# Optimization experiments

Measured on AMD Instinct MI355X. Metric: run time of the kernel, lower is better.

The kernel has to match this reference:

```python
import jax, jax.numpy as jnp
import numpy as np

N_TOK, BATCH, D, MEM, H, W = 196, 64, 256, 2048, 16, 16


def setup_inputs() -> dict:
    key = jax.random.key(0)
    ks = jax.random.split(key, 9)
    w_scale = 1.0 / np.sqrt(D)  # ~ Linear default init scale
    return {
        "input_tokens": jax.random.normal(ks[0], (N_TOK, BATCH, D), jnp.float32),
        "ch_memory": jax.random.normal(ks[1], (MEM, D), jnp.float32) * 0.1,
        "ch_wq": jax.random.normal(ks[2], (D, D), jnp.float32) * w_scale,
        "ch_wk": jax.random.normal(ks[3], (D, D), jnp.float32) * w_scale,
        "ch_wv": jax.random.normal(ks[4], (D, D), jnp.float32) * w_scale,
        "sp_memory": jax.random.normal(ks[5], (MEM, H, W), jnp.float32) * 0.1,
        "sp_wq": jax.random.normal(ks[6], (D, D), jnp.float32) * w_scale,
        "sp_wk": jax.random.normal(ks[7], (D, D), jnp.float32) * w_scale,
        "sp_wv": jax.random.normal(ks[8], (D, D), jnp.float32) * w_scale,
    }


def reference(input_tokens, ch_memory, ch_wq, ch_wk, ch_wv,
              sp_memory, sp_wq, sp_wk, sp_wv):
    n_tok, batch, d = input_tokens.shape
    hw = d  # spatial branch requires feature_dim == H*W
    x = input_tokens.reshape(n_tok * batch, d)  # [NB, D]

    # ---- Channel memory branch: dot-product softmax read ----
    q = x @ ch_wq.T                       # [NB, D]
    k = ch_memory @ ch_wk.T               # [M, D]
    v = ch_memory @ ch_wv.T               # [M, D]
    scores = (q @ k.T) * (1.0 / jnp.sqrt(jnp.float32(d)))  # [NB, M]
    att_c = jax.nn.softmax(scores, axis=-1)
    out_c = att_c @ v                     # [NB, D]

    # ---- Spatial memory branch: SSIM-score softmax read ----
    mem_flat = sp_memory.reshape(sp_memory.shape[0], hw)  # [M, HW]
    qf = x @ sp_wq.T                      # [NB, HW]
    kf = mem_flat @ sp_wk.T               # [M, HW]
    vf = mem_flat @ sp_wv.T               # [M, HW]

    q_mean = jnp.mean(qf, axis=1, keepdims=True)          # [NB, 1]
    k_mean = jnp.mean(kf, axis=1, keepdims=True)          # [M, 1]
    q_var = jnp.var(qf, axis=1, ddof=1, keepdims=True)    # unbiased, like torch.var
    k_var = jnp.var(kf, axis=1, ddof=1, keepdims=True)
    cov = ((qf - q_mean) @ (kf - k_mean).T) / jnp.float32(hw - 1)  # [NB, M]

    c1, c2 = 0.01, 0.03
    mean_prod = q_mean @ k_mean.T                          # [NB, M]
    numerator = (2.0 * mean_prod + c1) * (2.0 * cov + c2)
    denominator = (q_mean ** 2 + (k_mean.T) ** 2 + c1) * (q_var + k_var.T + c2)
    ssim = numerator / (denominator + 1e-8)                # [NB, M]

    att_s = jax.nn.softmax(ssim, axis=-1)
    out_s = att_s @ vf                     # [NB, HW] == [NB, D]

    return (out_c + out_s).reshape(n_tok, batch, d)
```

## Files before the change

kernel.cpp:

```cpp
#include <hip/hip_runtime.h>

#define NBQ 12544
#define DM  256
#define MM  2048

typedef __attribute__((ext_vector_type(8)))  __bf16 bf16x8;
typedef __attribute__((ext_vector_type(4)))  float  floatx4;

__device__ __forceinline__ ushort f2bf(float x) {
    unsigned u = __float_as_uint(x);
    u += 0x7fffu + ((u >> 16) & 1u);
    return (ushort)(u >> 16);
}
__device__ __forceinline__ float bf2f(ushort h) {
    return __uint_as_float(((unsigned)h) << 16);
}
__device__ __forceinline__ ushort4 cvt4(float4 f) {
    union { __bf16 h[4]; ushort4 u; } r;
    r.h[0] = (__bf16)f.x; r.h[1] = (__bf16)f.y;
    r.h[2] = (__bf16)f.z; r.h[3] = (__bf16)f.w;
    return r.u;
}

__device__ __forceinline__ void glds16(const ushort* g, ushort* l) {
    __builtin_amdgcn_global_load_lds(
        (const __attribute__((address_space(1))) unsigned int*)g,
        (__attribute__((address_space(3))) unsigned int*)l, 16, 0, 0);
}

#define WAITVM(N) asm volatile("s_waitcnt vmcnt(" #N ")" ::: "memory")
#define WAITLGKM0 asm volatile("s_waitcnt lgkmcnt(0)" ::: "memory")

__global__ __launch_bounds__(256) void gemm_proj_all(
    const float* __restrict__ x,      const float* __restrict__ ch_mem,
    const float* __restrict__ ch_wq,  const float* __restrict__ ch_wk,
    const float* __restrict__ ch_wv,  const float* __restrict__ sp_mem,
    const float* __restrict__ sp_wq,  const float* __restrict__ sp_wk,
    const float* __restrict__ sp_wv,
    ushort* __restrict__ Qb,  ushort* __restrict__ QFb,
    ushort* __restrict__ Kb,  ushort* __restrict__ KFb,
    ushort* __restrict__ Vtb, ushort* __restrict__ VFtb)
{
    __shared__ ushort As[64][72];
    __shared__ ushort W1s[64][72];
    __shared__ ushort W2s[64][72];

    int bid = blockIdx.x;
    const float* A; const float* W1; const float* W2;
    ushort* C1; ushort* C2; int nrows, trans2;
    if (bid < 784) {
        A = x; W1 = ch_wq; W2 = sp_wq; C1 = Qb; C2 = QFb; nrows = NBQ; trans2 = 0;
    } else if (bid < 912) {
        A = ch_mem; W1 = ch_wk; W2 = ch_wv; C1 = Kb; C2 = Vtb;
        nrows = MM; trans2 = 1; bid -= 784;
    } else {
        A = sp_mem; W1 = sp_wk; W2 = sp_wv; C1 = KFb; C2 = VFtb;
        nrows = MM; trans2 = 1; bid -= 912;
    }
    const int r0 = (bid >> 2) * 64;
    const int c0 = (bid & 3) * 64;

    const int tid  = threadIdx.x;
    const int wv   = tid >> 6;
    const int lane = tid & 63;
    const int quad = lane >> 4;
    const int l16  = lane & 15;
    const int rw = (wv & 1) * 32;
    const int cw = (wv >> 1) * 32;

    floatx4 acc1[2][2], acc2[2][2];
    #pragma unroll
    for (int i = 0; i < 2; ++i)
        #pragma unroll
        for (int j = 0; j < 2; ++j) {
            acc1[i][j] = (floatx4){0.f, 0.f, 0.f, 0.f};
            acc2[i][j] = (floatx4){0.f, 0.f, 0.f, 0.f};
        }

    float4 a4[4], w14[4], w24[4];
    #pragma unroll
    for (int it = 0; it < 4; ++it) {
        int idx = tid + it * 256;
        int r = idx >> 4, c4 = (idx & 15) * 4;
        a4[it]  = *(const float4*)(A  + (size_t)(r0 + r) * 256 + c4);
        w14[it] = *(const float4*)(W1 + (size_t)(c0 + r) * 256 + c4);
        w24[it] = *(const float4*)(W2 + (size_t)(c0 + r) * 256 + c4);
    }

    for (int d0 = 0; d0 < 256; d0 += 64) {
        __syncthreads();
        #pragma unroll
        for (int it = 0; it < 4; ++it) {
            int idx = tid + it * 256;
            int r = idx >> 4, c4 = (idx & 15) * 4;
            *(ushort4*)&As[r][c4]  = cvt4(a4[it]);
            *(ushort4*)&W1s[r][c4] = cvt4(w14[it]);
            *(ushort4*)&W2s[r][c4] = cvt4(w24[it]);
        }
        if (d0 + 64 < 256) {
            #pragma unroll
            for (int it = 0; it < 4; ++it) {
                int idx = tid + it * 256;
                int r = idx >> 4, c4 = (idx & 15) * 4;
                a4[it]  = *(const float4*)(A  + (size_t)(r0 + r) * 256 + d0 + 64 + c4);
                w14[it] = *(const float4*)(W1 + (size_t)(c0 + r) * 256 + d0 + 64 + c4);
                w24[it] = *(const float4*)(W2 + (size_t)(c0 + r) * 256 + d0 + 64 + c4);
            }
        }
        __syncthreads();
        #pragma unroll
        for (int kk = 0; kk < 64; kk += 32) {
            bf16x8 aA0 = *(const bf16x8*)&As[rw + l16][kk + quad * 8];
            bf16x8 aA1 = *(const bf16x8*)&As[rw + 16 + l16][kk + quad * 8];
            bf16x8 b10 = *(const bf16x8*)&W1s[cw + l16][kk + quad * 8];
            bf16x8 b11 = *(const bf16x8*)&W1s[cw + 16 + l16][kk + quad * 8];
            bf16x8 b20 = *(const bf16x8*)&W2s[cw + l16][kk + quad * 8];
            bf16x8 b21 = *(const bf16x8*)&W2s[cw + 16 + l16][kk + quad * 8];
            acc1[0][0] = __builtin_amdgcn_mfma_f32_16x16x32_bf16(aA0, b10, acc1[0][0], 0, 0, 0);
            acc1[0][1] = __builtin_amdgcn_mfma_f32_16x16x32_bf16(aA0, b11, acc1[0][1], 0, 0, 0);
            acc1[1][0] = __builtin_amdgcn_mfma_f32_16x16x32_bf16(aA1, b10, acc1[1][0], 0, 0, 0);
            acc1[1][1] = __builtin_amdgcn_mfma_f32_16x16x32_bf16(aA1, b11, acc1[1][1], 0, 0, 0);
            acc2[0][0] = __builtin_amdgcn_mfma_f32_16x16x32_bf16(aA0, b20, acc2[0][0], 0, 0, 0);
            acc2[0][1] = __builtin_amdgcn_mfma_f32_16x16x32_bf16(aA0, b21, acc2[0][1], 0, 0, 0);
            acc2[1][0] = __builtin_amdgcn_mfma_f32_16x16x32_bf16(aA1, b20, acc2[1][0], 0, 0, 0);
            acc2[1][1] = __builtin_amdgcn_mfma_f32_16x16x32_bf16(aA1, b21, acc2[1][1], 0, 0, 0);
        }
    }

    #pragma unroll
    for (int ag = 0; ag < 2; ++ag)
        #pragma unroll
        for (int cg = 0; cg < 2; ++cg)
            #pragma unroll
            for (int i = 0; i < 4; ++i)
                C1[(size_t)(r0 + rw + ag * 16 + quad * 4 + i) * 256
                   + c0 + cw + cg * 16 + l16] = f2bf(acc1[ag][cg][i]);

    if (!trans2) {
        #pragma unroll
        for (int ag = 0; ag < 2; ++ag)
            #pragma unroll
            for (int cg = 0; cg < 2; ++cg)
                #pragma unroll
                for (int i = 0; i < 4; ++i)
                    C2[(size_t)(r0 + rw + ag * 16 + quad * 4 + i) * 256
                       + c0 + cw + cg * 16 + l16] = f2bf(acc2[ag][cg][i]);
    } else {
        __syncthreads();
        #pragma unroll
        for (int ag = 0; ag < 2; ++ag)
            #pragma unroll
            for (int cg = 0; cg < 2; ++cg)
                #pragma unroll
                for (int i = 0; i < 4; ++i)
                    W2s[cw + cg * 16 + l16][rw + ag * 16 + quad * 4 + i] = f2bf(acc2[ag][cg][i]);
        __syncthreads();
        const int col = tid >> 2;
        const int seg = (tid & 3) * 16;
        #pragma unroll
        for (int j = 0; j < 2; ++j)
            *(uint4*)(C2 + (size_t)(c0 + col) * nrows + r0 + seg + j * 8) =
                *(const uint4*)&W2s[col][seg + j * 8];
    }
}

__global__ __launch_bounds__(256) void row_stats_kf(
    const ushort* __restrict__ KFb, float* __restrict__ km, float* __restrict__ kv)
{
    const int row  = blockIdx.x * 4 + (threadIdx.x >> 6);
    const int lane = threadIdx.x & 63;
    ushort4 u = *(const ushort4*)(KFb + (size_t)row * 256 + lane * 4);
    float a = bf2f(u.x), b = bf2f(u.y), c = bf2f(u.z), d = bf2f(u.w);
    float s  = a + b + c + d;
    float ss = a * a + b * b + c * c + d * d;
    #pragma unroll
    for (int off = 32; off > 0; off >>= 1) {
        s  += __shfl_down(s, off);
        ss += __shfl_down(ss, off);
    }
    if (lane == 0) {
        float m = s * (1.f / 256.f);
        km[row] = m;
        kv[row] = (ss - 256.f * m * m) * (1.f / 255.f) + 0.03f;
    }
}

#define STAGE_TILE(b, ti)                                                     \
    {                                                                         \
        const ushort* kp_ = kp0 + (size_t)(ti) * 32 * DM;                     \
        const ushort* vp_ = vp0 + (ti) * 32;                                  \
        ushort* dst_ = SMu + (b) * 16384;                                     \
        _Pragma("unroll")                                                     \
        for (int p = 0; p < 4; ++p) {                                         \
            int db = (wv * 4 + p) * 512;                                      \
            glds16(kp_ + offK[p], dst_ + db);                                 \
            glds16(vp_ + offV[p], dst_ + 8192 + db);                          \
        }                                                                     \
    }

__global__ __launch_bounds__(256, 2) void fused_attn_x4(
    const ushort* __restrict__ Qb,  const ushort* __restrict__ QFb,
    const ushort* __restrict__ Kb,  const ushort* __restrict__ KFb,
    const ushort* __restrict__ Vtb, const ushort* __restrict__ VFtb,
    const float* __restrict__ km_, const float* __restrict__ kv_,
    float* __restrict__ part, float* __restrict__ denp)
{
    __shared__ ushort SMu[32768];

    const int tid  = threadIdx.x;
    const int wv   = tid >> 6;
    const int lane = tid & 63;
    const int quad = lane >> 4;
    const int l16  = lane & 15;

    const int k8   = blockIdx.x & 7;
    const int j    = blockIdx.x >> 3;
    const int br   = (j >= 49) ? 1 : 0;
    const int half = k8 & 3;
    const int qc   = (k8 >> 2) * 49 + (br ? j - 49 : j);
    const int q0   = qc * 128;
    const int kbase = half * 512;
    const int NT   = 16;

    const ushort* qsrc = br ? QFb : Qb;
    const ushort* Ksel = br ? KFb : Kb;
    const ushort* Vsel = br ? VFtb : Vtb;

    bf16x8 aQ0[8], aQ1[8];
    {
        const ushort* qp = qsrc + (size_t)(q0 + wv * 32 + l16) * DM + quad * 8;
        #pragma unroll
        for (int s = 0; s < 8; ++s) {
            aQ0[s] = __builtin_nontemporal_load((const bf16x8*)(qp + s * 32));
            aQ1[s] = __builtin_nontemporal_load((const bf16x8*)(qp + 16 * DM + s * 32));
        }
    }

    float qmv0 = 0.f, qvv0 = 0.f, qmv1 = 0.f, qvv1 = 0.f, qm2_0 = 0.f, qm2_1 = 0.f;
    if (br) {
        float s0 = 0.f, ss0 = 0.f, s1 = 0.f, ss1 = 0.f;
        #pragma unroll
        for (int s = 0; s < 8; ++s)
            #pragma unroll
            for (int jj = 0; jj < 8; ++jj) {
                float v0 = (float)aQ0[s][jj], v1 = (float)aQ1[s][jj];
                s0 += v0; ss0 += v0 * v0; s1 += v1; ss1 += v1 * v1;
            }
        s0  += __shfl_xor(s0, 16, 64);  s0  += __shfl_xor(s0, 32, 64);
        ss0 += __shfl_xor(ss0, 16, 64); ss0 += __shfl_xor(ss0, 32, 64);
        s1  += __shfl_xor(s1, 16, 64);  s1  += __shfl_xor(s1, 32, 64);
        ss1 += __shfl_xor(ss1, 16, 64); ss1 += __shfl_xor(ss1, 32, 64);
        qmv0 = s0 * (1.f / 256.f);
        qvv0 = (ss0 - 256.f * qmv0 * qmv0) * (1.f / 255.f);
        qmv1 = s1 * (1.f / 256.f);
        qvv1 = (ss1 - 256.f * qmv1 * qmv1) * (1.f / 255.f);
        qm2_0 = qmv0 * qmv0 + 0.01f;
        qm2_1 = qmv1 * qmv1 + 0.01f;
    }

    int offK[4], offV[4];
    #pragma unroll
    for (int p = 0; p < 4; ++p) {
        int jw = wv * 4 + p;
        int Rk = 2 * jw + (lane >> 5);
        int rk = (Rk & 3) + ((Rk >> 4) & 1) * 4 + ((Rk >> 2) & 3) * 8;
        int ck = (lane & 31) ^ (Rk & 7);
        offK[p] = rk * DM + ck * 8;
        int Rv = 16 * jw + (lane >> 2);
        int cv = (lane & 3) ^ (Rv & 3);
        offV[p] = Rv * MM + cv * 8;
    }

    const ushort* kp0 = Ksel + (size_t)kbase * DM;
    const ushort* vp0 = Vsel + kbase;

    floatx4 acc0[16], acc1[16];
    #pragma unroll
    for (int t = 0; t < 16; ++t) {
        acc0[t] = (floatx4){0.f, 0.f, 0.f, 0.f};
        acc1[t] = (floatx4){0.f, 0.f, 0.f, 0.f};
    }
    float den0 = 0.f, den1 = 0.f;
    const int ksw  = l16 & 7;
    const int vswo = (quad ^ (l16 & 3)) * 8;

    floatx4 kmc0 = {0,0,0,0}, kmc1 = {0,0,0,0}, kvc0 = {0,0,0,0}, kvc1 = {0,0,0,0};

    STAGE_TILE(0, 0);
    if (br) {
        kmc0 = *(const floatx4*)(km_ + kbase + 8 * quad);
        kmc1 = *(const floatx4*)(km_ + kbase + 8 * quad + 4);
        kvc0 = *(const floatx4*)(kv_ + kbase + 8 * quad);
        kvc1 = *(const floatx4*)(kv_ + kbase + 8 * quad + 4);
    }

    int buf = 0;
    for (int ti = 0; ti < NT; ++ti) {
        const bool have_next = (ti + 1 < NT);
        floatx4 kmn0 = {0,0,0,0}, kmn1 = {0,0,0,0}, kvn0 = {0,0,0,0}, kvn1 = {0,0,0,0};
        if (have_next) {
            STAGE_TILE(buf ^ 1, ti + 1);
            if (br) {
                const int kk1 = kbase + (ti + 1) * 32;
                kmn0 = *(const floatx4*)(km_ + kk1 + 8 * quad);
                kmn1 = *(const floatx4*)(km_ + kk1 + 8 * quad + 4);
                kvn0 = *(const floatx4*)(kv_ + kk1 + 8 * quad);
                kvn1 = *(const floatx4*)(kv_ + kk1 + 8 * quad + 4);
            }
        }
        if (have_next) { if (br) WAITVM(12); else WAITVM(8); }
        else           { WAITVM(0); }
        __builtin_amdgcn_sched_barrier(0);
        __builtin_amdgcn_s_barrier();
        __builtin_amdgcn_sched_barrier(0);

        const ushort* Ks = SMu + buf * 16384;
        const ushort* Vs = Ks + 8192;

        floatx4 S00 = (floatx4){0.f, 0.f, 0.f, 0.f};
        floatx4 S10 = (floatx4){0.f, 0.f, 0.f, 0.f};
        floatx4 S01 = (floatx4){0.f, 0.f, 0.f, 0.f};
        floatx4 S11 = (floatx4){0.f, 0.f, 0.f, 0.f};
        #pragma unroll
        for (int s = 0; s < 8; ++s) {
            int off = ((s * 4 + quad) ^ ksw) * 8;
            bf16x8 aK0 = *(const bf16x8*)(Ks + l16 * DM + off);
            bf16x8 aK1 = *(const bf16x8*)(Ks + 4096 + l16 * DM + off);
            S00 = __builtin_amdgcn_mfma_f32_16x16x32_bf16(aK0, aQ0[s], S00, 0, 0, 0);
            S10 = __builtin_amdgcn_mfma_f32_16x16x32_bf16(aK1, aQ0[s], S10, 0, 0, 0);
            S01 = __builtin_amdgcn_mfma_f32_16x16x32_bf16(aK0, aQ1[s], S01, 0, 0, 0);
            S11 = __builtin_amdgcn_mfma_f32_16x16x32_bf16(aK1, aQ1[s], S11, 0, 0, 0);
        }

        float p0[8], p1[8];
        if (!br) {
            #pragma unroll
            for (int r = 0; r < 4; ++r) {
                p0[r]     = __expf(S00[r] * 0.0625f);
                p0[4 + r] = __expf(S10[r] * 0.0625f);
                p1[r]     = __expf(S01[r] * 0.0625f);
                p1[4 + r] = __expf(S11[r] * 0.0625f);
            }
        } else {
            #pragma unroll
            for (int r = 0; r < 4; ++r) {
                {
                    float kmr = kmc0[r];
                    float mp  = qmv0 * kmr;
                    float cov = (S00[r] - 256.f * mp) * (1.f / 255.f);
                    float num = (2.f * mp + 0.01f) * (2.f * cov + 0.03f);
                    float dn  = (qm2_0 + kmr * kmr) * (qvv0 + kvc0[r]) + 1e-8f;
                    p0[r] = __expf(num / dn);
                }
                {
                    float kmr = kmc1[r];
                    float mp  = qmv0 * kmr;
                    float cov = (S10[r] - 256.f * mp) * (1.f / 255.f);
                    float num = (2.f * mp + 0.01f) * (2.f * cov + 0.03f);
                    float dn  = (qm2_0 + kmr * kmr) * (qvv0 + kvc1[r]) + 1e-8f;
                    p0[4 + r] = __expf(num / dn);
                }
                {
                    float kmr = kmc0[r];
                    float mp  = qmv1 * kmr;
                    float cov = (S01[r] - 256.f * mp) * (1.f / 255.f);
                    float num = (2.f * mp + 0.01f) * (2.f * cov + 0.03f);
                    float dn  = (qm2_1 + kmr * kmr) * (qvv1 + kvc0[r]) + 1e-8f;
                    p1[r] = __expf(num / dn);
                }
                {
                    float kmr = kmc1[r];
                    float mp  = qmv1 * kmr;
                    float cov = (S11[r] - 256.f * mp) * (1.f / 255.f);
                    float num = (2.f * mp + 0.01f) * (2.f * cov + 0.03f);
                    float dn  = (qm2_1 + kmr * kmr) * (qvv1 + kvc1[r]) + 1e-8f;
                    p1[4 + r] = __expf(num / dn);
                }
            }
        }
        union { __bf16 h[8]; bf16x8 v; } ap0, ap1;
        #pragma unroll
        for (int jj = 0; jj < 8; ++jj) {
            den0 += p0[jj]; ap0.h[jj] = (__bf16)p0[jj];
            den1 += p1[jj]; ap1.h[jj] = (__bf16)p1[jj];
        }

        #pragma unroll
        for (int t = 0; t < 16; ++t) {
            bf16x8 bV = *(const bf16x8*)(Vs + (t * 16 + l16) * 32 + vswo);
            acc0[t] = __builtin_amdgcn_mfma_f32_16x16x32_bf16(ap0.v, bV, acc0[t], 0, 0, 0);
            acc1[t] = __builtin_amdgcn_mfma_f32_16x16x32_bf16(ap1.v, bV, acc1[t], 0, 0, 0);
        }

        WAITLGKM0;
        __builtin_amdgcn_sched_barrier(0);
        __builtin_amdgcn_s_barrier();
        __builtin_amdgcn_sched_barrier(0);

        kmc0 = kmn0; kmc1 = kmn1; kvc0 = kvn0; kvc1 = kvn1;
        buf ^= 1;
    }

    den0 += __shfl_xor(den0, 16, 64); den0 += __shfl_xor(den0, 32, 64);
    den1 += __shfl_xor(den1, 16, 64); den1 += __shfl_xor(den1, 32, 64);

    const int sec = br * 4 + half;
    float* Np = part + (size_t)sec * ((size_t)NBQ * DM);
    #pragma unroll
    for (int t = 0; t < 16; ++t)
        #pragma unroll
        for (int r = 0; r < 4; ++r) {
            int row = q0 + wv * 32 + quad * 4 + r;
            __builtin_nontemporal_store(acc0[t][r], &Np[(size_t)row * DM + t * 16 + l16]);
            __builtin_nontemporal_store(acc1[t][r], &Np[(size_t)(row + 16) * DM + t * 16 + l16]);
        }
    if (lane < 16) {
        denp[(size_t)sec * NBQ + q0 + wv * 32 + lane]      = den0;
        denp[(size_t)sec * NBQ + q0 + wv * 32 + 16 + lane] = den1;
    }
}

__global__ __launch_bounds__(256, 2) void fused_attn_fb(
    const ushort* __restrict__ Qb,  const ushort* __restrict__ QFb,
    const ushort* __restrict__ Kb,  const ushort* __restrict__ KFb,
    const ushort* __restrict__ Vtb, const ushort* __restrict__ VFtb,
    const float* __restrict__ km_, const float* __restrict__ kv_,
    float* __restrict__ out)
{
    __shared__ ushort SMu[32768];
    float* combuf = (float*)SMu;

    const int tid  = threadIdx.x;
    const int wv   = tid >> 6;
    const int lane = tid & 63;
    const int quad = lane >> 4;
    const int l16  = lane & 15;
    const int qsel = wv & 1;
    const int br   = wv >> 1;
    const int q0   = blockIdx.x * 32;

    const ushort* qsrc = br ? QFb : Qb;
    bf16x8 aQ[8];
    {
        const ushort* qp = qsrc + (size_t)(q0 + qsel * 16 + l16) * DM + quad * 8;
        #pragma unroll
        for (int s = 0; s < 8; ++s) aQ[s] = *(const bf16x8*)(qp + s * 32);
    }

    float qmv = 0.f, qvv = 0.f, qm2 = 0.f;
    if (br) {
        float sum = 0.f, ss = 0.f;
        #pragma unroll
        for (int s = 0; s < 8; ++s)
            #pragma unroll
            for (int jj = 0; jj < 8; ++jj) {
                float v = (float)aQ[s][jj];
                sum += v; ss += v * v;
            }
        sum += __shfl_xor(sum, 16, 64); sum += __shfl_xor(sum, 32, 64);
        ss  += __shfl_xor(ss, 16, 64);  ss  += __shfl_xor(ss, 32, 64);
        qmv = sum * (1.f / 256.f);
        qvv = (ss - 256.f * qmv * qmv) * (1.f / 255.f);
        qm2 = qmv * qmv + 0.01f;
    }

    int offK[4], offV[4];
    #pragma unroll
    for (int p = 0; p < 4; ++p) {
        int jw = wv * 4 + p;
        int Rk = 2 * jw + (lane >> 5);
        int rk = (Rk & 3) + ((Rk >> 4) & 1) * 4 + ((Rk >> 2) & 3) * 8;
        int ck = (lane & 31) ^ (Rk & 7);
        offK[p] = rk * DM + ck * 8;
        int Rv = 16 * jw + (lane >> 2);
        int cv = (lane & 3) ^ (Rv & 3);
        offV[p] = Rv * MM + cv * 8;
    }

    const ushort* kp  = Kb;
    const ushort* kfp = KFb;
    const ushort* vp  = Vtb;
    const ushort* vfp = VFtb;

    floatx4 acc[16];
    #pragma unroll
    for (int t = 0; t < 16; ++t) acc[t] = (floatx4){0.f, 0.f, 0.f, 0.f};
    float den = 0.f;

    const int ksw  = l16 & 7;
    const int vswo = (quad ^ (l16 & 3)) * 8;

    for (int kt = 0; kt < MM; kt += 32) {
        __syncthreads();
        #pragma unroll
        for (int p = 0; p < 4; ++p) {
            int db = (wv * 4 + p) * 512;
            glds16(kp  + offK[p], SMu + db);
            glds16(kfp + offK[p], SMu + 8192 + db);
            glds16(vp  + offV[p], SMu + 16384 + db);
            glds16(vfp + offV[p], SMu + 24576 + db);
        }
        kp += 32 * DM; kfp += 32 * DM; vp += 32; vfp += 32;
        __syncthreads();

        const ushort* Ks = SMu + (br ? 8192 : 0);
        floatx4 S0 = (floatx4){0.f, 0.f, 0.f, 0.f};
        floatx4 S1 = (floatx4){0.f, 0.f, 0.f, 0.f};
        #pragma unroll
        for (int s = 0; s < 8; ++s) {
            int off = ((s * 4 + quad) ^ ksw) * 8;
            bf16x8 aK0 = *(const bf16x8*)(Ks + l16 * DM + off);
            bf16x8 aK1 = *(const bf16x8*)(Ks + 4096 + l16 * DM + off);
            S0 = __builtin_amdgcn_mfma_f32_16x16x32_bf16(aK0, aQ[s], S0, 0, 0, 0);
            S1 = __builtin_amdgcn_mfma_f32_16x16x32_bf16(aK1, aQ[s], S1, 0, 0, 0);
        }

        float pb[8];
        if (!br) {
            #pragma unroll
            for (int r = 0; r < 4; ++r) {
                pb[r]     = __expf(S0[r] * 0.0625f);
                pb[4 + r] = __expf(S1[r] * 0.0625f);
            }
        } else {
            floatx4 km0 = *(const floatx4*)(km_ + kt + 8 * quad);
            floatx4 km1 = *(const floatx4*)(km_ + kt + 8 * quad + 4);
            floatx4 kv0 = *(const floatx4*)(kv_ + kt + 8 * quad);
            floatx4 kv1 = *(const floatx4*)(kv_ + kt + 8 * quad + 4);
            #pragma unroll
            for (int r = 0; r < 4; ++r) {
                {
                    float kmr = km0[r];
                    float mp  = qmv * kmr;
                    float cov = (S0[r] - 256.f * mp) * (1.f / 255.f);
                    float num = (2.f * mp + 0.01f) * (2.f * cov + 0.03f);
                    float dn  = (qm2 + kmr * kmr) * (qvv + kv0[r]) + 1e-8f;
                    pb[r] = __expf(num / dn);
                }
                {
                    float kmr = km1[r];
                    float mp  = qmv * kmr;
                    float cov = (S1[r] - 256.f * mp) * (1.f / 255.f);
                    float num = (2.f * mp + 0.01f) * (2.f * cov + 0.03f);
                    float dn  = (qm2 + kmr * kmr) * (qvv + kv1[r]) + 1e-8f;
                    pb[4 + r] = __expf(num / dn);
                }
            }
        }
        union { __bf16 h[8]; bf16x8 v; } ap;
        #pragma unroll
        for (int jj = 0; jj < 8; ++jj) {
            den += pb[jj];
            ap.h[jj] = (__bf16)pb[jj];
        }

        const ushort* Vs = SMu + (br ? 24576 : 16384);
        #pragma unroll
        for (int t = 0; t < 16; ++t) {
            bf16x8 bV = *(const bf16x8*)(Vs + (t * 16 + l16) * 32 + vswo);
            acc[t] = __builtin_amdgcn_mfma_f32_16x16x32_bf16(ap.v, bV, acc[t], 0, 0, 0);
        }
    }

    den += __shfl_xor(den, 16, 64);
    den += __shfl_xor(den, 32, 64);
    float rdn[4];
    #pragma unroll
    for (int r = 0; r < 4; ++r)
        rdn[r] = 1.f / __shfl(den, quad * 4 + r, 64);

    __syncthreads();
    if (br) {
        #pragma unroll
        for (int t = 0; t < 16; ++t)
            #pragma unroll
            for (int r = 0; r < 4; ++r)
                combuf[(qsel * 16 + quad * 4 + r) * 256 + t * 16 + l16] = acc[t][r] * rdn[r];
    }
    __syncthreads();
    if (!br) {
        #pragma unroll
        for (int t = 0; t < 16; ++t)
            #pragma unroll
            for (int r = 0; r < 4; ++r) {
                int ql = qsel * 16 + quad * 4 + r;
                out[(size_t)(q0 + ql) * DM + t * 16 + l16] =
                    acc[t][r] * rdn[r] + combuf[ql * 256 + t * 16 + l16];
            }
    }
}

__global__ __launch_bounds__(256) void combine_halves(
    const float* __restrict__ part, const float* __restrict__ denp,
    float* __restrict__ out)
{
    const size_t stride = (size_t)NBQ * 64;
    const floatx4* p4 = (const floatx4*)part;
    floatx4* o4 = (floatx4*)out;
    #pragma unroll
    for (int u = 0; u < 2; ++u) {
        size_t i = (size_t)blockIdx.x * 512 + (size_t)u * 256 + threadIdx.x;
        int q = (int)(i >> 6);
        float dc = 0.f, ds = 0.f;
        #pragma unroll
        for (int h = 0; h < 4; ++h) {
            dc += denp[(size_t)h * NBQ + q];
            ds += denp[(size_t)(4 + h) * NBQ + q];
        }
        float rc = 1.f / dc, rs = 1.f / ds;
        floatx4 nc = {0.f, 0.f, 0.f, 0.f}, ns = {0.f, 0.f, 0.f, 0.f};
        #pragma unroll
        for (int h = 0; h < 4; ++h) {
            floatx4 c = __builtin_nontemporal_load(&p4[(size_t)h * stride + i]);
            floatx4 s = __builtin_nontemporal_load(&p4[(size_t)(4 + h) * stride + i]);
            nc += c;
            ns += s;
        }
        o4[i] = nc * rc + ns * rs;
    }
}

extern "C" void kernel_launch(void* const* d_in, const int* in_sizes, int n_in,
                              void* d_out, int out_size, void* d_ws, size_t ws_size,
                              hipStream_t stream)
{
    const float* x      = (const float*)d_in[0];
    const float* ch_mem = (const float*)d_in[1];
    const float* ch_wq  = (const float*)d_in[2];
    const float* ch_wk  = (const float*)d_in[3];
    const float* ch_wv  = (const float*)d_in[4];
    const float* sp_mem = (const float*)d_in[5];
    const float* sp_wq  = (const float*)d_in[6];
    const float* sp_wk  = (const float*)d_in[7];
    const float* sp_wv  = (const float*)d_in[8];
    float* out = (float*)d_out;

    ushort* Qb   = (ushort*)d_ws;
    ushort* QFb  = Qb   + (size_t)NBQ * DM;
    ushort* Kb   = QFb  + (size_t)NBQ * DM;
    ushort* KFb  = Kb   + (size_t)MM * DM;
    ushort* Vtb  = KFb  + (size_t)MM * DM;
    ushort* VFtb = Vtb  + (size_t)MM * DM;
    float*  km   = (float*)(VFtb + (size_t)MM * DM);
    float*  kv   = km + MM;
    float*  denp = kv + MM;
    float*  part = denp + (size_t)8 * NBQ;

    const size_t base_b = (size_t)((char*)part - (char*)d_ws);
    const size_t need4  = base_b + (size_t)8 * NBQ * DM * sizeof(float);

    dim3 blk(256);
    gemm_proj_all<<<dim3(1040), blk, 0, stream>>>(
        x, ch_mem, ch_wq, ch_wk, ch_wv, sp_mem, sp_wq, sp_wk, sp_wv,
        Qb, QFb, Kb, KFb, Vtb, VFtb);
    row_stats_kf<<<dim3(MM / 4), blk, 0, stream>>>(KFb, km, kv);
    if (ws_size >= need4) {
        fused_attn_x4<<<dim3(784), blk, 0, stream>>>(
            Qb, QFb, Kb, KFb, Vtb, VFtb, km, kv, part, denp);
        combine_halves<<<dim3(NBQ * DM / 4 / 512), blk, 0, stream>>>(part, denp, out);
    } else {
        fused_attn_fb<<<dim3(NBQ / 32), blk, 0, stream>>>(
            Qb, QFb, Kb, KFb, Vtb, VFtb, km, kv, out);
    }
}
```

Baseline: 306.7 us.

## Add bf16 pre-conversion projection GEMM and simplify attention kernel pipelining

Adds a kernel that converts inputs and weights to bf16 up front, and a new double-buffered projection GEMM that streams bf16 tiles into LDS with async global-to-LDS loads. It also reworks the attention kernel into a templated version. That version uses a different block-to-work mapping, plain __syncthreads instead of hand-tuned vmcnt waits and a single barrier per tile, per-tile loads of km/kv instead of prefetching them, and regular rather than nontemporal loads and stores. The conversion pass adds extra memory traffic and a launch. The simpler synchronisation may lose some load/compute overlap in the attention kernel, which dominates runtime.

```diff
diff --git a/kernel.cpp b/kernel.cpp
--- a/kernel.cpp
+++ b/kernel.cpp
@@ -28,8 +28,169 @@
         (__attribute__((address_space(3))) unsigned int*)l, 16, 0, 0);
 }
 
-#define WAITVM(N) asm volatile("s_waitcnt vmcnt(" #N ")" ::: "memory")
-#define WAITLGKM0 asm volatile("s_waitcnt lgkmcnt(0)" ::: "memory")
+__global__ __launch_bounds__(256) void cvt_all_bf16(
+    const float* __restrict__ x,   const float* __restrict__ ch_mem,
+    const float* __restrict__ sp_mem,
+    const float* __restrict__ cwq, const float* __restrict__ swq,
+    const float* __restrict__ cwk, const float* __restrict__ cwv,
+    const float* __restrict__ swk, const float* __restrict__ swv,
+    ushort* __restrict__ xb, ushort* __restrict__ cmb,
+    ushort* __restrict__ smb, ushort* __restrict__ wb)
+{
+    int bid = blockIdx.x;
+    const float* src; ushort* dst; size_t off;
+    if (bid < 392)      { src = x;      dst = xb;  off = (size_t)bid * 8192; }
+    else if (bid < 456) { src = ch_mem; dst = cmb; off = (size_t)(bid - 392) * 8192; }
+    else if (bid < 520) { src = sp_mem; dst = smb; off = (size_t)(bid - 456) * 8192; }
+    else {
+        int w = bid - 520, wi = w >> 3;
+        if      (wi == 0) src = cwq;
+        else if (wi == 1) src = swq;
+        else if (wi == 2) src = cwk;
+        else if (wi == 3) src = cwv;
+        else if (wi == 4) src = swk;
+        else              src = swv;
+        dst = wb + (size_t)wi * 65536;
+        off = (size_t)(w & 7) * 8192;
+    }
+    #pragma unroll
+    for (int i = 0; i < 4; ++i) {
+        size_t b = off + (size_t)i * 2048 + (size_t)threadIdx.x * 8;
+        float4 a0 = *(const float4*)(src + b);
+        float4 a1 = *(const float4*)(src + b + 4);
+        *(ushort4*)(dst + b)     = cvt4(a0);
+        *(ushort4*)(dst + b + 4) = cvt4(a1);
+    }
+}
+
+#define PSTG(b, d0_)                                                          \
+    { _Pragma("unroll") for (int p = 0; p < 2; ++p) {                         \
+        int j = wv * 2 + p;                                                   \
+        int R = j * 8 + (lane >> 3);                                          \
+        int so = R * 256 + (d0_) + (((lane & 7) ^ (R & 7)) << 3);             \
+        int doff = j * 512;                                                   \
+        glds16(As_ + so, &SM[b][0][0][0] + doff);                             \
+        glds16(W1_ + so, &SM[b][1][0][0] + doff);                             \
+        glds16(W2_ + so, &SM[b][2][0][0] + doff);                             \
+    } }
+
+__global__ __launch_bounds__(256, 2) void gemm_proj_bf16(
+    const ushort* __restrict__ xb,  const ushort* __restrict__ cmb,
+    const ushort* __restrict__ smb, const ushort* __restrict__ wb,
+    ushort* __restrict__ Qb,  ushort* __restrict__ QFb,
+    ushort* __restrict__ Kb,  ushort* __restrict__ KFb,
+    ushort* __restrict__ Vtb, ushort* __restrict__ VFtb)
+{
+    __shared__ ushort SM[2][3][64][64];
+
+    int bid = blockIdx.x;
+    const ushort* A; const ushort* W1; const ushort* W2;
+    ushort* C1; ushort* C2; int nrows, trans2;
+    if (bid < 784) {
+        A = xb; W1 = wb; W2 = wb + 65536; C1 = Qb; C2 = QFb; nrows = NBQ; trans2 = 0;
+    } else if (bid < 912) {
+        A = cmb; W1 = wb + 2 * 65536; W2 = wb + 3 * 65536; C1 = Kb; C2 = Vtb;
+        nrows = MM; trans2 = 1; bid -= 784;
+    } else {
+        A = smb; W1 = wb + 4 * 65536; W2 = wb + 5 * 65536; C1 = KFb; C2 = VFtb;
+        nrows = MM; trans2 = 1; bid -= 912;
+    }
+    const int r0 = (bid >> 2) * 64;
+    const int c0 = (bid & 3) * 64;
+
+    const int tid  = threadIdx.x;
+    const int wv   = tid >> 6;
+    const int lane = tid & 63;
+    const int quad = lane >> 4;
+    const int l16  = lane & 15;
+    const int rw = (wv & 1) * 32;
+    const int cw = (wv >> 1) * 32;
+
+    const ushort* As_ = A  + (size_t)r0 * 256;
+    const ushort* W1_ = W1 + (size_t)c0 * 256;
+    const ushort* W2_ = W2 + (size_t)c0 * 256;
+
+    floatx4 acc1[2][2], acc2[2][2];
+    #pragma unroll
+    for (int i = 0; i < 2; ++i)
+        #pragma unroll
+        for (int j = 0; j < 2; ++j) {
+            acc1[i][j] = (floatx4){0.f, 0.f, 0.f, 0.f};
+            acc2[i][j] = (floatx4){0.f, 0.f, 0.f, 0.f};
+        }
+
+    PSTG(0, 0);
+    __syncthreads();
+
+    int buf = 0;
+    const int kx = l16 & 7;
+    for (int d0 = 0; d0 < 256; d0 += 64) {
+        if (d0 + 64 < 256) PSTG(buf ^ 1, d0 + 64);
+        #pragma unroll
+        for (int kk = 0; kk < 64; kk += 32) {
+            int off = (((kk >> 3) + quad) ^ kx) << 3;
+            bf16x8 aA0 = *(const bf16x8*)&SM[buf][0][rw + l16][off];
+            bf16x8 aA1 = *(const bf16x8*)&SM[buf][0][rw + 16 + l16][off];
+            bf16x8 b10 = *(const bf16x8*)&SM[buf][1][cw + l16][off];
+            bf16x8 b11 = *(const bf16x8*)&SM[buf][1][cw + 16 + l16][off];
+            bf16x8 b20 = *(const bf16x8*)&SM[buf][2][cw + l16][off];
+            bf16x8 b21 = *(const bf16x8*)&SM[buf][2][cw + 16 + l16][off];
+            acc1[0][0] = __builtin_amdgcn_mfma_f32_16x16x32_bf16(aA0, b10, acc1[0][0], 0, 0, 0);
+            acc1[0][1] = __builtin_amdgcn_mfma_f32_16x16x32_bf16(aA0, b11, acc1[0][1], 0, 0, 0);
+            acc1[1][0] = __builtin_amdgcn_mfma_f32_16x16x32_bf16(aA1, b10, acc1[1][0], 0, 0, 0);
+            acc1[1][1] = __builtin_amdgcn_mfma_f32_16x16x32_bf16(aA1, b11, acc1[1][1], 0, 0, 0);
+            acc2[0][0] = __builtin_amdgcn_mfma_f32_16x16x32_bf16(aA0, b20, acc2[0][0], 0, 0, 0);
+            acc2[0][1] = __builtin_amdgcn_mfma_f32_16x16x32_bf16(aA0, b21, acc2[0][1], 0, 0, 0);
+            acc2[1][0] = __builtin_amdgcn_mfma_f32_16x16x32_bf16(aA1, b20, acc2[1][0], 0, 0, 0);
+            acc2[1][1] = __builtin_amdgcn_mfma_f32_16x16x32_bf16(aA1, b21, acc2[1][1], 0, 0, 0);
+        }
+        __syncthreads();
+        buf ^= 1;
+    }
+
+    #pragma unroll
+    for (int ag = 0; ag < 2; ++ag)
+        #pragma unroll
+        for (int cg = 0; cg < 2; ++cg)
+            #pragma unroll
+            for (int i = 0; i < 4; ++i)
+                C1[(size_t)(r0 + rw + ag * 16 + quad * 4 + i) * 256
+                   + c0 + cw + cg * 16 + l16] = f2bf(acc1[ag][cg][i]);
+
+    if (!trans2) {
+        #pragma unroll
+        for (int ag = 0; ag < 2; ++ag)
+            #pragma unroll
+            for (int cg = 0; cg < 2; ++cg)
+                #pragma unroll
+                for (int i = 0; i < 4; ++i)
+                    C2[(size_t)(r0 + rw + ag * 16 + quad * 4 + i) * 256
+                       + c0 + cw + cg * 16 + l16] = f2bf(acc2[ag][cg][i]);
+    } else {
+        __syncthreads();
+        ushort (*W2s)[64] = SM[0][2];
+        #pragma unroll
+        for (int ag = 0; ag < 2; ++ag)
+            #pragma unroll
+            for (int cg = 0; cg < 2; ++cg)
+                #pragma unroll
+                for (int i = 0; i < 4; ++i) {
+                    int col = rw + ag * 16 + quad * 4 + i;
+                    int R   = cw + cg * 16 + l16;
+                    W2s[R][(((col >> 3) ^ (R & 7)) << 3) + (col & 7)] =
+                        f2bf(acc2[ag][cg][i]);
+                }
+        __syncthreads();
+        const int col = tid >> 2;
+        const int cj0 = (tid & 3) * 2;
+        #pragma unroll
+        for (int j = 0; j < 2; ++j) {
+            int oc = cj0 + j;
+            *(uint4*)(C2 + (size_t)(c0 + col) * nrows + r0 + oc * 8) =
+                *(const uint4*)&W2s[col][(oc ^ (col & 7)) << 3];
+        }
+    }
+}
 
 __global__ __launch_bounds__(256) void gemm_proj_all(
     const float* __restrict__ x,      const float* __restrict__ ch_mem,
@@ -198,7 +359,8 @@
         }                                                                     \
     }
 
-__global__ __launch_bounds__(256, 2) void fused_attn_x4(
+template<int NHALF>
+__global__ __launch_bounds__(256, 2) void fused_attn_1br(
     const ushort* __restrict__ Qb,  const ushort* __restrict__ QFb,
     const ushort* __restrict__ Kb,  const ushort* __restrict__ KFb,
     const ushort* __restrict__ Vtb, const ushort* __restrict__ VFtb,
@@ -213,14 +375,16 @@
     const int quad = lane >> 4;
     const int l16  = lane & 15;
 
-    const int k8   = blockIdx.x & 7;
-    const int j    = blockIdx.x >> 3;
-    const int br   = (j >= 49) ? 1 : 0;
-    const int half = k8 & 3;
-    const int qc   = (k8 >> 2) * 49 + (br ? j - 49 : j);
+    const int NQC = NBQ / 128;
+    const int per_br = NQC * NHALF;
+    int bid = blockIdx.x;
+    const int br  = (bid < per_br) ? 1 : 0;
+    int rem = br ? bid : bid - per_br;
+    const int half = rem / NQC;
+    const int qc   = rem - half * NQC;
     const int q0   = qc * 128;
-    const int kbase = half * 512;
-    const int NT   = 16;
+    const int kbase = half * (MM / NHALF);
+    const int NT   = (MM / NHALF) / 32;
 
     const ushort* qsrc = br ? QFb : Qb;
     const ushort* Ksel = br ? KFb : Kb;
@@ -231,19 +395,19 @@
         const ushort* qp = qsrc + (size_t)(q0 + wv * 32 + l16) * DM + quad * 8;
         #pragma unroll
         for (int s = 0; s < 8; ++s) {
-            aQ0[s] = __builtin_nontemporal_load((const bf16x8*)(qp + s * 32));
-            aQ1[s] = __builtin_nontemporal_load((const bf16x8*)(qp + 16 * DM + s * 32));
-        }
-    }
-
-    float qmv0 = 0.f, qvv0 = 0.f, qmv1 = 0.f, qvv1 = 0.f, qm2_0 = 0.f, qm2_1 = 0.f;
+            aQ0[s] = *(const bf16x8*)(qp + s * 32);
+            aQ1[s] = *(const bf16x8*)(qp + 16 * DM + s * 32);
+        }
+    }
+
+    float qmv0 = 0.f, qvv0 = 0.f, qmv1 = 0.f, qvv1 = 0.f, qm20 = 0.f, qm21 = 0.f;
     if (br) {
         float s0 = 0.f, ss0 = 0.f, s1 = 0.f, ss1 = 0.f;
         #pragma unroll
         for (int s = 0; s < 8; ++s)
             #pragma unroll
-            for (int jj = 0; jj < 8; ++jj) {
-                float v0 = (float)aQ0[s][jj], v1 = (float)aQ1[s][jj];
+            for (int j = 0; j < 8; ++j) {
+                float v0 = (float)aQ0[s][j], v1 = (float)aQ1[s][j];
                 s0 += v0; ss0 += v0 * v0; s1 += v1; ss1 += v1 * v1;
             }
         s0  += __shfl_xor(s0, 16, 64);  s0  += __shfl_xor(s0, 32, 64);
@@ -254,19 +418,19 @@
         qvv0 = (ss0 - 256.f * qmv0 * qmv0) * (1.f / 255.f);
         qmv1 = s1 * (1.f / 256.f);
         qvv1 = (ss1 - 256.f * qmv1 * qmv1) * (1.f / 255.f);
-        qm2_0 = qmv0 * qmv0 + 0.01f;
-        qm2_1 = qmv1 * qmv1 + 0.01f;
+        qm20 = qmv0 * qmv0 + 0.01f;
+        qm21 = qmv1 * qmv1 + 0.01f;
     }
 
     int offK[4], offV[4];
     #pragma unroll
     for (int p = 0; p < 4; ++p) {
-        int jw = wv * 4 + p;
-        int Rk = 2 * jw + (lane >> 5);
+        int j  = wv * 4 + p;
+        int Rk = 2 * j + (lane >> 5);
         int rk = (Rk & 3) + ((Rk >> 4) & 1) * 4 + ((Rk >> 2) & 3) * 8;
         int ck = (lane & 31) ^ (Rk & 7);
         offK[p] = rk * DM + ck * 8;
-        int Rv = 16 * jw + (lane >> 2);
+        int Rv = 16 * j + (lane >> 2);
         int cv = (lane & 3) ^ (Rv & 3);
         offV[p] = Rv * MM + cv * 8;
     }
@@ -284,35 +448,12 @@
     const int ksw  = l16 & 7;
     const int vswo = (quad ^ (l16 & 3)) * 8;
 
-    floatx4 kmc0 = {0,0,0,0}, kmc1 = {0,0,0,0}, kvc0 = {0,0,0,0}, kvc1 = {0,0,0,0};
-
     STAGE_TILE(0, 0);
-    if (br) {
-        kmc0 = *(const floatx4*)(km_ + kbase + 8 * quad);
-        kmc1 = *(const floatx4*)(km_ + kbase + 8 * quad + 4);
-        kvc0 = *(const floatx4*)(kv_ + kbase + 8 * quad);
-        kvc1 = *(const floatx4*)(kv_ + kbase + 8 * quad + 4);
-    }
+    __syncthreads();
 
     int buf = 0;
     for (int ti = 0; ti < NT; ++ti) {
-        const bool have_next = (ti + 1 < NT);
-        floatx4 kmn0 = {0,0,0,0}, kmn1 = {0,0,0,0}, kvn0 = {0,0,0,0}, kvn1 = {0,0,0,0};
-        if (have_next) {
-            STAGE_TILE(buf ^ 1, ti + 1);
-            if (br) {
-                const int kk1 = kbase + (ti + 1) * 32;
-                kmn0 = *(const floatx4*)(km_ + kk1 + 8 * quad);
-                kmn1 = *(const floatx4*)(km_ + kk1 + 8 * quad + 4);
-                kvn0 = *(const floatx4*)(kv_ + kk1 + 8 * quad);
-                kvn1 = *(const floatx4*)(kv_ + kk1 + 8 * quad + 4);
-            }
-        }
-        if (have_next) { if (br) WAITVM(12); else WAITVM(8); }
-        else           { WAITVM(0); }
-        __builtin_amdgcn_sched_barrier(0);
-        __builtin_amdgcn_s_barrier();
-        __builtin_amdgcn_sched_barrier(0);
+        if (ti + 1 < NT) STAGE_TILE(buf ^ 1, ti + 1);
 
         const ushort* Ks = SMu + buf * 16384;
         const ushort* Vs = Ks + 8192;
@@ -332,6 +473,7 @@
             S11 = __builtin_amdgcn_mfma_f32_16x16x32_bf16(aK1, aQ1[s], S11, 0, 0, 0);
         }
 
+        const int kk = kbase + ti * 32;
         float p0[8], p1[8];
         if (!br) {
             #pragma unroll
@@ -342,47 +484,51 @@
                 p1[4 + r] = __expf(S11[r] * 0.0625f);
             }
         } else {
+            floatx4 km0 = *(const floatx4*)(km_ + kk + 8 * quad);
+            floatx4 km1 = *(const floatx4*)(km_ + kk + 8 * quad + 4);
+            floatx4 kv0 = *(const floatx4*)(kv_ + kk + 8 * quad);
+            floatx4 kv1 = *(const floatx4*)(kv_ + kk + 8 * quad + 4);
             #pragma unroll
             for (int r = 0; r < 4; ++r) {
                 {
-                    float kmr = kmc0[r];
+                    float kmr = km0[r];
                     float mp  = qmv0 * kmr;
                     float cov = (S00[r] - 256.f * mp) * (1.f / 255.f);
                     float num = (2.f * mp + 0.01f) * (2.f * cov + 0.03f);
-                    float dn  = (qm2_0 + kmr * kmr) * (qvv0 + kvc0[r]) + 1e-8f;
+                    float dn  = (qm20 + kmr * kmr) * (qvv0 + kv0[r]) + 1e-8f;
                     p0[r] = __expf(num / dn);
                 }
                 {
-                    float kmr = kmc1[r];
+                    float kmr = km1[r];
                     float mp  = qmv0 * kmr;
                     float cov = (S10[r] - 256.f * mp) * (1.f / 255.f);
                     float num = (2.f * mp + 0.01f) * (2.f * cov + 0.03f);
-                    float dn  = (qm2_0 + kmr * kmr) * (qvv0 + kvc1[r]) + 1e-8f;
+                    float dn  = (qm20 + kmr * kmr) * (qvv0 + kv1[r]) + 1e-8f;
                     p0[4 + r] = __expf(num / dn);
                 }
                 {
-                    float kmr = kmc0[r];
+                    float kmr = km0[r];
                     float mp  = qmv1 * kmr;
                     float cov = (S01[r] - 256.f * mp) * (1.f / 255.f);
                     float num = (2.f * mp + 0.01f) * (2.f * cov + 0.03f);
-                    float dn  = (qm2_1 + kmr * kmr) * (qvv1 + kvc0[r]) + 1e-8f;
+                    float dn  = (qm21 + kmr * kmr) * (qvv1 + kv0[r]) + 1e-8f;
                     p1[r] = __expf(num / dn);
                 }
                 {
-                    float kmr = kmc1[r];
+                    float kmr = km1[r];
                     float mp  = qmv1 * kmr;
                     float cov = (S11[r] - 256.f * mp) * (1.f / 255.f);
                     float num = (2.f * mp + 0.01f) * (2.f * cov + 0.03f);
-                    float dn  = (qm2_1 + kmr * kmr) * (qvv1 + kvc1[r]) + 1e-8f;
+                    float dn  = (qm21 + kmr * kmr) * (qvv1 + kv1[r]) + 1e-8f;
                     p1[4 + r] = __expf(num / dn);
                 }
             }
         }
         union { __bf16 h[8]; bf16x8 v; } ap0, ap1;
         #pragma unroll
-        for (int jj = 0; jj < 8; ++jj) {
-            den0 += p0[jj]; ap0.h[jj] = (__bf16)p0[jj];
-            den1 += p1[jj]; ap1.h[jj] = (__bf16)p1[jj];
+        for (int j = 0; j < 8; ++j) {
+            den0 += p0[j]; ap0.h[j] = (__bf16)p0[j];
+            den1 += p1[j]; ap1.h[j] = (__bf16)p1[j];
         }
 
         #pragma unroll
@@ -392,27 +538,22 @@
             acc1[t] = __builtin_amdgcn_mfma_f32_16x16x32_bf16(ap1.v, bV, acc1[t], 0, 0, 0);
         }
 
-        WAITLGKM0;
-        __builtin_amdgcn_sched_barrier(0);
-        __builtin_amdgcn_s_barrier();
-        __builtin_amdgcn_sched_barrier(0);
-
-        kmc0 = kmn0; kmc1 = kmn1; kvc0 = kvn0; kvc1 = kvn1;
+        __syncthreads();
         buf ^= 1;
     }
 
     den0 += __shfl_xor(den0, 16, 64); den0 += __shfl_xor(den0, 32, 64);
     den1 += __shfl_xor(den1, 16, 64); den1 += __shfl_xor(den1, 32, 64);
 
-    const int sec = br * 4 + half;
+    const int sec = br * NHALF + half;
     float* Np = part + (size_t)sec * ((size_t)NBQ * DM);
     #pragma unroll
     for (int t = 0; t < 16; ++t)
         #pragma unroll
         for (int r = 0; r < 4; ++r) {
             int row = q0 + wv * 32 + quad * 4 + r;
-            __builtin_nontemporal_store(acc0[t][r], &Np[(size_t)row * DM + t * 16 + l16]);
-            __builtin_nontemporal_store(acc1[t][r], &Np[(size_t)(row + 16) * DM + t * 16 + l16]);
+            Np[(size_t)row * DM + t * 16 + l16]        = acc0[t][r];
+            Np[(size_t)(row + 16) * DM + t * 16 + l16] = acc1[t][r];
         }
     if (lane < 16) {
         denp[(size_t)sec * NBQ + q0 + wv * 32 + lane]      = den0;
@@ -645,17 +786,29 @@
     float*  kv   = km + MM;
     float*  denp = kv + MM;
     float*  part = denp + (size_t)8 * NBQ;
-
-    const size_t base_b = (size_t)((char*)part - (char*)d_ws);
-    const size_t need4  = base_b + (size_t)8 * NBQ * DM * sizeof(float);
+    ushort* xb   = (ushort*)(part + (size_t)8 * NBQ * DM);
+    ushort* cmb  = xb  + (size_t)NBQ * DM;
+    ushort* smb  = cmb + (size_t)MM * DM;
+    ushort* wb   = smb + (size_t)MM * DM;
+
+    const size_t need4 = (size_t)((char*)xb - (char*)d_ws);
+    const size_t need5 = (size_t)((char*)(wb + (size_t)6 * DM * DM) - (char*)d_ws);
 
     dim3 blk(256);
-    gemm_proj_all<<<dim3(1040), blk, 0, stream>>>(
-        x, ch_mem, ch_wq, ch_wk, ch_wv, sp_mem, sp_wq, sp_wk, sp_wv,
-        Qb, QFb, Kb, KFb, Vtb, VFtb);
+    if (ws_size >= need5) {
+        cvt_all_bf16<<<dim3(568), blk, 0, stream>>>(
+            x, ch_mem, sp_mem, ch_wq, sp_wq, ch_wk, ch_wv, sp_wk, sp_wv,
+            xb, cmb, smb, wb);
+        gemm_proj_bf16<<<dim3(1040), blk, 0, stream>>>(
+            xb, cmb, smb, wb, Qb, QFb, Kb, KFb, Vtb, VFtb);
+    } else {
+        gemm_proj_all<<<dim3(1040), blk, 0, stream>>>(
+            x, ch_mem, ch_wq, ch_wk, ch_wv, sp_mem, sp_wq, sp_wk, sp_wv,
+            Qb, QFb, Kb, KFb, Vtb, VFtb);
+    }
     row_stats_kf<<<dim3(MM / 4), blk, 0, stream>>>(KFb, km, kv);
     if (ws_size >= need4) {
-        fused_attn_x4<<<dim3(784), blk, 0, stream>>>(
+        fused_attn_1br<4><<<dim3(784), blk, 0, stream>>>(
             Qb, QFb, Kb, KFb, Vtb, VFtb, km, kv, part, denp);
         combine_halves<<<dim3(NBQ * DM / 4 / 512), blk, 0, stream>>>(part, denp, out);
     } else {
```

Result: faster. 256.8 us (-16.3%).
